# Optimization experiments

Hardware: AMD Instinct MI355X
Metric: run time of the kernel (lower is better)

The kernel has to match this reference:

```python
import jax, jax.numpy as jnp
import numpy as np

J, H, MAXREL = 24, 8, 49  # num_joints, temporal heads, max_relative_position


def _pos_encoding(seq_len, d_model):
    pos = jnp.arange(seq_len, dtype=jnp.float32)[:, None]
    i = jnp.arange(d_model, dtype=jnp.float32)[None, :]
    angle = pos / jnp.power(10000.0, 2.0 * jnp.floor(i / 2.0) / d_model)
    return jnp.where(jnp.arange(d_model)[None, :] % 2 == 0, jnp.sin(angle), jnp.cos(angle))  # [S, D]


def _rel_index(seq_len):
    r = jnp.arange(seq_len)
    dist = jnp.clip(r[None, :] - r[:, None], -MAXREL, MAXREL) + MAXREL
    return dist  # [S, S] int


def setup_inputs() -> dict:
    key = jax.random.key(0)
    ks = jax.random.split(key, 12)
    B, S, D = 32, 120, 128
    depth = D // H
    s = 0.02
    x = jax.random.normal(ks[0], (B, S, J, D), dtype=jnp.float32)
    mask = jnp.triu(jnp.ones((1, 1, S, S), dtype=jnp.float32), k=1)  # look-ahead mask
    Wq = jax.random.normal(ks[1], (J, D, D), dtype=jnp.float32) * s
    bq = jnp.zeros((J, D), dtype=jnp.float32)
    Wk = jax.random.normal(ks[2], (J, D, D), dtype=jnp.float32) * s
    bk = jnp.zeros((J, D), dtype=jnp.float32)
    Wv = jax.random.normal(ks[3], (J, D, D), dtype=jnp.float32) * s
    bv = jnp.zeros((J, D), dtype=jnp.float32)
    Wo = jax.random.normal(ks[4], (D, D), dtype=jnp.float32) * s
    bo = jnp.zeros((D,), dtype=jnp.float32)
    key_table = jax.random.normal(ks[5], (2 * MAXREL + 1, depth), dtype=jnp.float32) * s
    val_table = jax.random.normal(ks[6], (2 * MAXREL + 1, depth), dtype=jnp.float32) * s
    return {"x": x, "mask": mask, "Wq": Wq, "bq": bq, "Wk": Wk, "bk": bk,
            "Wv": Wv, "bv": bv, "Wo": Wo, "bo": bo,
            "key_table": key_table, "val_table": val_table}


def reference(x, mask, Wq, bq, Wk, bk, Wv, bv, Wo, bo, key_table, val_table):
    B, S, _, D = x.shape
    depth = D // H
    # absolute positional encoding, broadcast over batch and joints
    x = x + _pos_encoding(S, D)[None, :, None, :]
    xj = jnp.transpose(x, (2, 0, 1, 3))  # [J, B, S, D]
    # per-joint linear projections (torch Linear: y = x @ W^T + b)
    q = jnp.einsum('jbsd,jed->jbse', xj, Wq) + bq[:, None, None, :]
    k = jnp.einsum('jbsd,jed->jbse', xj, Wk) + bk[:, None, None, :]
    v = jnp.einsum('jbsd,jed->jbse', xj, Wv) + bv[:, None, None, :]
    # split heads -> [J, B, H, S, depth]
    split = lambda t: t.reshape(J, B, S, H, depth).transpose(0, 1, 3, 2, 4)
    q, k, v = split(q), split(k), split(v)
    # relative key/value embeddings [S, S, depth]
    rel = _rel_index(S)
    rk = key_table[rel]
    rv = val_table[rel]
    logits = jnp.einsum('jbhsd,jbhtd->jbhst', q, k) + jnp.einsum('jbhsd,std->jbhst', q, rk)
    logits = logits / jnp.float32(np.sqrt(depth)) + mask * (-1e9)
    w = jax.nn.softmax(logits, axis=-1)  # [J, B, H, S, T]
    out = jnp.einsum('jbhst,jbhtd->jbhsd', w, v) + jnp.einsum('jbhst,std->jbhsd', w, rv)
    out = out.transpose(0, 1, 3, 2, 4).reshape(J, B, S, D)  # merge heads
    out = jnp.einsum('jbsd,ed->jbse', out, Wo) + bo  # shared output projection
    outputs = out.transpose(1, 2, 0, 3)  # [B, S, J, D]
    attn_weights = w[..., -1, :].transpose(1, 0, 2, 3)  # [B, J, H, T]
    return outputs, attn_weights
```

## Files before the change

### kernel.cpp

```cpp
#include <hip/hip_runtime.h>
#include <math.h>

#define Jn 24
#define Bn 32
#define Sn 120
#define Dn 128
#define Hn 8
#define DEP 16
#define ALD 136

#define QSCL 0.36067376022224085f

typedef _Float16 f16x8 __attribute__((ext_vector_type(8)));
typedef float f32x4 __attribute__((ext_vector_type(4)));

#if __has_builtin(__builtin_amdgcn_exp2f)
#define EXP2(x) __builtin_amdgcn_exp2f(x)
#else
#define EXP2(x) exp2f(x)
#endif

__global__ void pe_kernel(float* __restrict__ pe) {
    const int s = blockIdx.x, d = threadIdx.x;
    const float expo = (float)(2 * (d >> 1)) / (float)Dn;
    const float base = powf(10000.0f, -expo);
    const float ang = (float)s * base;
    pe[s * Dn + d] = (d & 1) ? cosf(ang) : sinf(ang);
}

__global__ __launch_bounds__(256)
void qkv_gemm(const float* __restrict__ x, const float* __restrict__ pe,
              const float* __restrict__ Wq, const float* __restrict__ bq,
              const float* __restrict__ Wk, const float* __restrict__ bk,
              const float* __restrict__ Wv, const float* __restrict__ bv,
              _Float16* __restrict__ qg, _Float16* __restrict__ kg,
              _Float16* __restrict__ vg, int jbase)
{
    extern __shared__ _Float16 lsu[];
    _Float16* As = lsu;
    _Float16* Bs = lsu + 128 * ALD;

    const int bid = blockIdx.x;
    const int mt = bid % 30;
    const int jc = bid / 30;
    const int j = jbase + jc;
    const int tid = threadIdx.x;

    for (int idx = tid; idx < 128 * 32; idx += 256) {
        const int r = idx >> 5;
        const int c = (idx & 31) << 2;
        const int mflat = mt * 128 + r;
        const int b = mflat / Sn;
        const int s = mflat % Sn;
        const float4 xv = *(const float4*)(x + (((size_t)(b * Sn + s)) * Jn + j) * Dn + c);
        const float4 pv = *(const float4*)(pe + s * Dn + c);
        _Float16* dst = As + r * ALD + c;
        dst[0] = (_Float16)(xv.x + pv.x); dst[1] = (_Float16)(xv.y + pv.y);
        dst[2] = (_Float16)(xv.z + pv.z); dst[3] = (_Float16)(xv.w + pv.w);
    }

    const int wid = tid >> 6;
    const int lane = tid & 63;
    const int wm = wid >> 1, wn = wid & 1;
    const int g = lane >> 4, q16 = lane & 15;

    for (int nt = 0; nt < 3; ++nt) {
        const float* Wsel = (nt == 0 ? Wq : (nt == 1 ? Wk : Wv)) + (size_t)j * Dn * Dn;
        const float* bsel = (nt == 0 ? bq : (nt == 1 ? bk : bv)) + (size_t)j * Dn;
        _Float16* obuf = (nt == 0 ? qg : (nt == 1 ? kg : vg));
        const float scl = (nt == 0) ? QSCL : 1.0f;

        if (nt) __syncthreads();
        for (int idx = tid; idx < 128 * 32; idx += 256) {
            const int e = idx >> 5;
            const int c = (idx & 31) << 2;
            const float4 wv = *(const float4*)(Wsel + (size_t)e * Dn + c);
            _Float16* dst = Bs + e * ALD + c;
            dst[0] = (_Float16)wv.x; dst[1] = (_Float16)wv.y;
            dst[2] = (_Float16)wv.z; dst[3] = (_Float16)wv.w;
        }
        __syncthreads();

        f32x4 acc[4][4];
        #pragma unroll
        for (int a = 0; a < 4; ++a)
            #pragma unroll
            for (int c2 = 0; c2 < 4; ++c2) acc[a][c2] = (f32x4){0.f, 0.f, 0.f, 0.f};

        #pragma unroll
        for (int ks = 0; ks < 4; ++ks) {
            const int kof = ks * 32 + g * 8;
            f16x8 av[4], bvf[4];
            #pragma unroll
            for (int fr = 0; fr < 4; ++fr)
                av[fr] = *(const f16x8*)(As + (wm * 64 + fr * 16 + q16) * ALD + kof);
            #pragma unroll
            for (int fc = 0; fc < 4; ++fc)
                bvf[fc] = *(const f16x8*)(Bs + (wn * 64 + fc * 16 + q16) * ALD + kof);
            #pragma unroll
            for (int fr = 0; fr < 4; ++fr)
                #pragma unroll
                for (int fc = 0; fc < 4; ++fc)
                    acc[fr][fc] = __builtin_amdgcn_mfma_f32_16x16x32_f16(av[fr], bvf[fc], acc[fr][fc], 0, 0, 0);
        }

        #pragma unroll
        for (int fc = 0; fc < 4; ++fc) {
            const int e = wn * 64 + fc * 16 + q16;
            const float be = bsel[e];
            const int h = e >> 4, ed = e & 15;
            #pragma unroll
            for (int fr = 0; fr < 4; ++fr) {
                #pragma unroll
                for (int r = 0; r < 4; ++r) {
                    const int mflat = mt * 128 + wm * 64 + fr * 16 + g * 4 + r;
                    const int b = mflat / Sn, s = mflat % Sn;
                    obuf[((size_t)((jc * Bn + b) * Hn + h)) * (Sn * DEP) + s * DEP + ed] =
                        (_Float16)((acc[fr][fc][r] + be) * scl);
                }
            }
        }
    }
}

#define AB_LD  184
#define QR_LD  52
#define A_VCT  0
#define A_RKT  5888
#define A_RV0  8960
#define A_ABUF 9024
#define A_QRB  32576
#define A_BYTES 39264

__global__ __launch_bounds__(256)
void attn_mfma(const _Float16* __restrict__ qg, const _Float16* __restrict__ kg,
               const _Float16* __restrict__ vg,
               const float* __restrict__ ktab, const float* __restrict__ vtab,
               _Float16* __restrict__ out_pre, float* __restrict__ attn_w, int jbase)
{
    extern __shared__ char smc[];
    _Float16* vct = (_Float16*)(smc + A_VCT);
    _Float16* rkt = (_Float16*)(smc + A_RKT);
    float*    rv0 = (float*)(smc + A_RV0);

    const int tid = threadIdx.x;
    const int wid = tid >> 6;
    const int lane = tid & 63;
    const int l15 = lane & 15;
    const int g = lane >> 4;
    const int bh = blockIdx.x;
    const int jc = bh >> 8;
    const int b = (bh >> 3) & 31;
    const int h = bh & 7;
    const int j = jbase + jc;

    _Float16* ab  = (_Float16*)(smc + A_ABUF) + wid * 16 * AB_LD;
    _Float16* qrb = (_Float16*)(smc + A_QRB) + wid * 16 * QR_LD;

    {
        unsigned* z = (unsigned*)smc;
        for (int idx = tid; idx < A_BYTES / 4; idx += 256) z[idx] = 0;
    }
    __syncthreads();
    const unsigned* vs = (const unsigned*)vg + (size_t)bh * 960;
    unsigned short* vctu = (unsigned short*)vct;
    for (int idx = tid; idx < 960; idx += 256) {
        const int s = idx >> 3, ep = idx & 7;
        const unsigned u = vs[idx];
        vctu[(2 * ep) * AB_LD + s] = (unsigned short)(u & 0xffffu);
        vctu[(2 * ep + 1) * AB_LD + s] = (unsigned short)(u >> 16);
    }
    for (int idx = tid; idx < 800; idx += 256) {
        const int d = idx >> 4, e = idx & 15;
        vct[e * AB_LD + 120 + d] = (_Float16)(vtab[d * DEP + e] - vtab[e]);
    }
    for (int idx = tid; idx < 800; idx += 256) {
        const int d = idx >> 4, e = idx & 15;
        rkt[d * 24 + e] = (_Float16)ktab[d * DEP + e];
    }
    if (tid < 16) rv0[tid] = vtab[tid];
    __syncthreads();

    const _Float16* qgu = qg + (size_t)bh * 1920;
    const _Float16* kgu = kg + (size_t)bh * 1920;
    _Float16* opre = out_pre + ((size_t)((j * Bn + b) * Hn + h)) * (Sn * DEP);

    const f16x8 zf = {0, 0, 0, 0, 0, 0, 0, 0};
    const f32x4 z4 = {0.f, 0.f, 0.f, 0.f};
    const float rv0f = rv0[l15];

    #pragma unroll
    for (int half = 0; half < 2; ++half) {
        const int m = half ? (7 - wid) : wid;

        const f16x8 afr = (g < 2) ? *(const f16x8*)(qgu + (16 * m + l15) * 16 + g * 8) : zf;
        f32x4 qr[4];
        #pragma unroll
        for (int n = 0; n < 4; ++n) {
            const f16x8 bfr = (g < 2) ? *(const f16x8*)(rkt + (16 * n + l15) * 24 + g * 8) : zf;
            qr[n] = __builtin_amdgcn_mfma_f32_16x16x32_f16(afr, bfr, z4, 0, 0, 0);
        }
        f32x4 acc[8];
        #pragma unroll
        for (int n = 0; n < 8; ++n) {
            if (n > m) break;
            const f16x8 bfr = (g < 2) ? *(const f16x8*)(kgu + (16 * n + l15) * 16 + g * 8) : zf;
            acc[n] = __builtin_amdgcn_mfma_f32_16x16x32_f16(afr, bfr, z4, 0, 0, 0);
        }
        #pragma unroll
        for (int n = 0; n < 4; ++n)
            #pragma unroll
            for (int r = 0; r < 4; ++r)
                if (n < 3 || l15 < 4)
                    qrb[(g * 4 + r) * QR_LD + 16 * n + l15] = (_Float16)qr[n][r];

        float rs[4];
        #pragma unroll
        for (int r = 0; r < 4; ++r) {
            const int row = g * 4 + r;
            const int srow = 16 * m + row;
            const int rowbase = row * AB_LD;
            const _Float16* qrow = qrb + row * QR_LD;
            const float qr0 = (float)qrow[0];
            float pv[8];
            float tot = 0.f;
            #pragma unroll
            for (int n = 0; n < 8; ++n) {
                if (n > m) break;
                float p;
                if (n <= m - 4) {
                    p = EXP2(acc[n][r] + qr0);
                } else if (n < m) {
                    int dist = 16 * (n - m) + 49 + l15 - row;
                    if (n == m - 3) dist = dist < 0 ? 0 : dist;
                    p = EXP2(acc[n][r] + (float)qrow[dist]);
                } else {
                    const int dist = 49 + l15 - row;
                    p = (l15 <= row) ? EXP2(acc[n][r] + (float)qrow[dist]) : 0.f;
                }
                pv[n] = p;
                tot += p;
                if (n < 7 || l15 < 8)
                    ab[rowbase + 16 * n + l15] = (_Float16)p;
            }
            #pragma unroll
            for (int mk = 1; mk < 16; mk <<= 1) tot += __shfl_xor(tot, mk);
            rs[r] = tot;

            #pragma unroll
            for (int n = 0; n < 8; ++n) {
                if (n < m - 3 || n > m) continue;
                const int dist = 16 * (n - m) + 49 + l15 - row;
                bool st = true;
                if (n == m - 3) st = (dist >= 1);
                if (n == m)     st = (l15 <= row);
                if (st) ab[rowbase + 120 + dist] = (_Float16)pv[n];
            }
            if (srow == Sn - 1) {
                const float inv = __builtin_amdgcn_rcpf(tot);
                #pragma unroll
                for (int n = 0; n < 8; ++n) {
                    if (n > m) break;
                    const int t = 16 * n + l15;
                    if (t < Sn)
                        attn_w[(((size_t)(b * Jn + j)) * Hn + h) * Sn + t] = pv[n] * inv;
                }
            }
        }

        f32x4 oacc = z4;
        #pragma unroll
        for (int kt = 0; kt < 3; ++kt) {
            if (kt > (m >> 1)) break;
            const f16x8 aw = *(const f16x8*)(ab + l15 * AB_LD + kt * 32 + g * 8);
            const f16x8 bv = *(const f16x8*)(vct + l15 * AB_LD + kt * 32 + g * 8);
            oacc = __builtin_amdgcn_mfma_f32_16x16x32_f16(aw, bv, oacc, 0, 0, 0);
        }
        #pragma unroll
        for (int kt = 3; kt < 5; ++kt) {
            const f16x8 aw = *(const f16x8*)(ab + l15 * AB_LD + kt * 32 + g * 8);
            const f16x8 bv = *(const f16x8*)(vct + l15 * AB_LD + kt * 32 + g * 8);
            oacc = __builtin_amdgcn_mfma_f32_16x16x32_f16(aw, bv, oacc, 0, 0, 0);
        }
        {
            const f16x8 aw = (g < 2) ? *(const f16x8*)(ab + l15 * AB_LD + 160 + g * 8) : zf;
            const f16x8 bv = (g < 2) ? *(const f16x8*)(vct + l15 * AB_LD + 160 + g * 8) : zf;
            oacc = __builtin_amdgcn_mfma_f32_16x16x32_f16(aw, bv, oacc, 0, 0, 0);
        }
        #pragma unroll
        for (int r = 0; r < 4; ++r) {
            const int srow = 16 * m + g * 4 + r;
            if (srow < Sn) {
                const float inv = __builtin_amdgcn_rcpf(rs[r]);
                opre[srow * DEP + l15] = (_Float16)(fmaf(oacc[r], inv, rv0f));
            }
        }
    }
}

__global__ __launch_bounds__(256)
void oproj_gemm(const _Float16* __restrict__ Ain, const float* __restrict__ Wo,
                const float* __restrict__ bo, float* __restrict__ out)
{
    extern __shared__ _Float16 lsu[];
    _Float16* As = lsu;
    _Float16* Bs = lsu + 128 * ALD;
    const int tid = threadIdx.x;
    const int mt = blockIdx.x;

    for (int idx = tid; idx < 128 * 8; idx += 256) {
        const int r = idx >> 3;
        const int h = idx & 7;
        const int mflat = mt * 128 + r;
        const int j = mflat / (Bn * Sn);
        const int rem = mflat % (Bn * Sn);
        const int b = rem / Sn, s = rem % Sn;
        const _Float16* src = Ain + (((size_t)(j * Bn + b) * Hn + h) * Sn + s) * DEP;
        *(uint4*)(As + r * ALD + h * 16)     = *(const uint4*)(src);
        *(uint4*)(As + r * ALD + h * 16 + 8) = *(const uint4*)(src + 8);
    }
    for (int idx = tid; idx < 128 * 32; idx += 256) {
        const int e = idx >> 5;
        const int c = (idx & 31) << 2;
        const float4 wv = *(const float4*)(Wo + (size_t)e * Dn + c);
        _Float16* dst = Bs + e * ALD + c;
        dst[0] = (_Float16)wv.x; dst[1] = (_Float16)wv.y;
        dst[2] = (_Float16)wv.z; dst[3] = (_Float16)wv.w;
    }
    __syncthreads();

    const int wid = tid >> 6;
    const int lane = tid & 63;
    const int wm = wid >> 1, wn = wid & 1;
    const int g = lane >> 4, q16 = lane & 15;

    f32x4 acc[4][4];
    #pragma unroll
    for (int a = 0; a < 4; ++a)
        #pragma unroll
        for (int c2 = 0; c2 < 4; ++c2) acc[a][c2] = (f32x4){0.f, 0.f, 0.f, 0.f};

    #pragma unroll
    for (int ks = 0; ks < 4; ++ks) {
        const int kof = ks * 32 + g * 8;
        f16x8 av[4], bvf[4];
        #pragma unroll
        for (int fr = 0; fr < 4; ++fr)
            av[fr] = *(const f16x8*)(As + (wm * 64 + fr * 16 + q16) * ALD + kof);
        #pragma unroll
        for (int fc = 0; fc < 4; ++fc)
            bvf[fc] = *(const f16x8*)(Bs + (wn * 64 + fc * 16 + q16) * ALD + kof);
        #pragma unroll
        for (int fr = 0; fr < 4; ++fr)
            #pragma unroll
            for (int fc = 0; fc < 4; ++fc)
                acc[fr][fc] = __builtin_amdgcn_mfma_f32_16x16x32_f16(av[fr], bvf[fc], acc[fr][fc], 0, 0, 0);
    }

    #pragma unroll
    for (int fc = 0; fc < 4; ++fc) {
        const int e = wn * 64 + fc * 16 + q16;
        const float be = bo[e];
        #pragma unroll
        for (int fr = 0; fr < 4; ++fr) {
            #pragma unroll
            for (int r = 0; r < 4; ++r) {
                const int m = mt * 128 + wm * 64 + fr * 16 + g * 4 + r;
                const int jj = m / (Bn * Sn);
                const int rem = m % (Bn * Sn);
                const int bb = rem / Sn, ss = rem % Sn;
                out[((size_t)(bb * Sn + ss) * Jn + jj) * Dn + e] = acc[fr][fc][r] + be;
            }
        }
    }
}

extern "C" void kernel_launch(void* const* d_in, const int* in_sizes, int n_in,
                              void* d_out, int out_size, void* d_ws, size_t ws_size,
                              hipStream_t stream)
{
    const float* x    = (const float*)d_in[0];
    const float* Wq   = (const float*)d_in[2];
    const float* bq   = (const float*)d_in[3];
    const float* Wk   = (const float*)d_in[4];
    const float* bk   = (const float*)d_in[5];
    const float* Wv   = (const float*)d_in[6];
    const float* bv   = (const float*)d_in[7];
    const float* Wo   = (const float*)d_in[8];
    const float* bo   = (const float*)d_in[9];
    const float* ktab = (const float*)d_in[10];
    const float* vtab = (const float*)d_in[11];

    float* out    = (float*)d_out;
    float* attn_w = out + (size_t)Bn * Sn * Jn * Dn;

    const size_t fullE = (size_t)Jn * Bn * Sn * Dn;
    int JCr = 24;
    {
        const size_t need = 65536 + 2 * (3 * fullE + fullE);
        if (ws_size < need) JCr = 6;
    }
    const size_t csz = (size_t)JCr * Bn * Hn * Sn * DEP;

    float* pe = (float*)d_ws;
    char* base = (char*)d_ws;
    _Float16* qg = (_Float16*)(base + 65536);
    _Float16* kg = qg + csz;
    _Float16* vg = kg + csz;
    _Float16* out_pre = vg + csz;

    pe_kernel<<<Sn, Dn, 0, stream>>>(pe);
    const int gemm_lds = 2 * 128 * ALD * 2;
    for (int c = 0; c < Jn; c += JCr) {
        qkv_gemm<<<JCr * 30, 256, gemm_lds, stream>>>(
            x, pe, Wq, bq, Wk, bk, Wv, bv, qg, kg, vg, c);
        attn_mfma<<<JCr * Bn * Hn, 256, A_BYTES, stream>>>(
            qg, kg, vg, ktab, vtab, out_pre, attn_w, c);
    }
    oproj_gemm<<<(Jn * Bn * Sn) / 128, 256, gemm_lds, stream>>>(out_pre, Wo, bo, out);
}
```

Before: 244.2 us.

## Process four batch-head units per attention block with register prefetch of next unit

Each attention block now loops over four (j,b,h) units instead of one. The per-block setup (LDS zeroing, relative-table staging) is amortized across units. Q, K and V loads for the next unit are issued into registers during the current unit's compute to hide global latency. This costs extra registers for the prefetched fragments, adds per-unit barriers and an ab re-zero, and launches four times fewer blocks.

```diff
diff --git a/kernel.cpp b/kernel.cpp
--- a/kernel.cpp
+++ b/kernel.cpp
@@ -8,6 +8,7 @@
 #define Hn 8
 #define DEP 16
 #define ALD 136
+#define UPB 4
 
 #define QSCL 0.36067376022224085f
 
@@ -148,28 +149,16 @@
     const int lane = tid & 63;
     const int l15 = lane & 15;
     const int g = lane >> 4;
-    const int bh = blockIdx.x;
-    const int jc = bh >> 8;
-    const int b = (bh >> 3) & 31;
-    const int h = bh & 7;
-    const int j = jbase + jc;
 
     _Float16* ab  = (_Float16*)(smc + A_ABUF) + wid * 16 * AB_LD;
     _Float16* qrb = (_Float16*)(smc + A_QRB) + wid * 16 * QR_LD;
+    unsigned short* vctu = (unsigned short*)vct;
 
     {
         unsigned* z = (unsigned*)smc;
         for (int idx = tid; idx < A_BYTES / 4; idx += 256) z[idx] = 0;
     }
     __syncthreads();
-    const unsigned* vs = (const unsigned*)vg + (size_t)bh * 960;
-    unsigned short* vctu = (unsigned short*)vct;
-    for (int idx = tid; idx < 960; idx += 256) {
-        const int s = idx >> 3, ep = idx & 7;
-        const unsigned u = vs[idx];
-        vctu[(2 * ep) * AB_LD + s] = (unsigned short)(u & 0xffffu);
-        vctu[(2 * ep + 1) * AB_LD + s] = (unsigned short)(u >> 16);
-    }
     for (int idx = tid; idx < 800; idx += 256) {
         const int d = idx >> 4, e = idx & 15;
         vct[e * AB_LD + 120 + d] = (_Float16)(vtab[d * DEP + e] - vtab[e]);
@@ -181,121 +170,168 @@
     if (tid < 16) rv0[tid] = vtab[tid];
     __syncthreads();
 
-    const _Float16* qgu = qg + (size_t)bh * 1920;
-    const _Float16* kgu = kg + (size_t)bh * 1920;
-    _Float16* opre = out_pre + ((size_t)((j * Bn + b) * Hn + h)) * (Sn * DEP);
-
+    const float rv0f = rv0[l15];
     const f16x8 zf = {0, 0, 0, 0, 0, 0, 0, 0};
     const f32x4 z4 = {0.f, 0.f, 0.f, 0.f};
-    const float rv0f = rv0[l15];
-
-    #pragma unroll
-    for (int half = 0; half < 2; ++half) {
-        const int m = half ? (7 - wid) : wid;
-
-        const f16x8 afr = (g < 2) ? *(const f16x8*)(qgu + (16 * m + l15) * 16 + g * 8) : zf;
-        f32x4 qr[4];
-        #pragma unroll
-        for (int n = 0; n < 4; ++n) {
-            const f16x8 bfr = (g < 2) ? *(const f16x8*)(rkt + (16 * n + l15) * 24 + g * 8) : zf;
-            qr[n] = __builtin_amdgcn_mfma_f32_16x16x32_f16(afr, bfr, z4, 0, 0, 0);
-        }
-        f32x4 acc[8];
-        #pragma unroll
-        for (int n = 0; n < 8; ++n) {
-            if (n > m) break;
-            const f16x8 bfr = (g < 2) ? *(const f16x8*)(kgu + (16 * n + l15) * 16 + g * 8) : zf;
-            acc[n] = __builtin_amdgcn_mfma_f32_16x16x32_f16(afr, bfr, z4, 0, 0, 0);
-        }
-        #pragma unroll
-        for (int n = 0; n < 4; ++n)
-            #pragma unroll
-            for (int r = 0; r < 4; ++r)
-                if (n < 3 || l15 < 4)
-                    qrb[(g * 4 + r) * QR_LD + 16 * n + l15] = (_Float16)qr[n][r];
-
-        float rs[4];
-        #pragma unroll
-        for (int r = 0; r < 4; ++r) {
-            const int row = g * 4 + r;
-            const int srow = 16 * m + row;
-            const int rowbase = row * AB_LD;
-            const _Float16* qrow = qrb + row * QR_LD;
-            const float qr0 = (float)qrow[0];
-            float pv[8];
-            float tot = 0.f;
+
+    unsigned pvw0, pvw1, pvw2, pvw3;
+    f16x8 afr0, afr1, kf[8];
+
+#define PREFETCH_UNIT(BH_) do {                                                     \
+        const unsigned* vsrc = (const unsigned*)vg + (size_t)(BH_) * 960;           \
+        pvw0 = vsrc[tid]; pvw1 = vsrc[tid + 256]; pvw2 = vsrc[tid + 512];           \
+        pvw3 = (tid < 192) ? vsrc[tid + 768] : 0u;                                  \
+        const _Float16* qn = qg + (size_t)(BH_) * 1920;                             \
+        const _Float16* kn = kg + (size_t)(BH_) * 1920;                             \
+        afr0 = (g < 2) ? *(const f16x8*)(qn + (16 * wid + l15) * 16 + g * 8) : zf;  \
+        afr1 = (g < 2) ? *(const f16x8*)(qn + (16 * (7 - wid) + l15) * 16 + g * 8) : zf; \
+        _Pragma("unroll")                                                           \
+        for (int nn = 0; nn < 8; ++nn) {                                            \
+            if (nn > 7 - wid) break;                                                \
+            kf[nn] = (g < 2) ? *(const f16x8*)(kn + (16 * nn + l15) * 16 + g * 8) : zf; \
+        }                                                                           \
+    } while (0)
+
+    int bh = blockIdx.x * UPB;
+    PREFETCH_UNIT(bh);
+
+    for (int u = 0; u < UPB; ++u, ++bh) {
+        const int jc = bh >> 8;
+        const int b = (bh >> 3) & 31;
+        const int h = bh & 7;
+        const int j = jbase + jc;
+        _Float16* opre = out_pre + ((size_t)((j * Bn + b) * Hn + h)) * (Sn * DEP);
+
+        {
+            int idx = tid;
+            #pragma unroll
+            for (int k2 = 0; k2 < 4; ++k2, idx += 256) {
+                const unsigned uu = (k2 == 0) ? pvw0 : (k2 == 1) ? pvw1 : (k2 == 2) ? pvw2 : pvw3;
+                if (idx < 960) {
+                    const int s = idx >> 3, ep = idx & 7;
+                    vctu[(2 * ep) * AB_LD + s] = (unsigned short)(uu & 0xffffu);
+                    vctu[(2 * ep + 1) * AB_LD + s] = (unsigned short)(uu >> 16);
+                }
+            }
+        }
+        __syncthreads();
+
+        #pragma unroll
+        for (int half = 0; half < 2; ++half) {
+            const int m = half ? (7 - wid) : wid;
+            const f16x8 afr = half ? afr1 : afr0;
+
+            f32x4 qr[4];
+            #pragma unroll
+            for (int n = 0; n < 4; ++n) {
+                const f16x8 bfr = (g < 2) ? *(const f16x8*)(rkt + (16 * n + l15) * 24 + g * 8) : zf;
+                qr[n] = __builtin_amdgcn_mfma_f32_16x16x32_f16(afr, bfr, z4, 0, 0, 0);
+            }
+            f32x4 acc[8];
             #pragma unroll
             for (int n = 0; n < 8; ++n) {
                 if (n > m) break;
-                float p;
-                if (n <= m - 4) {
-                    p = EXP2(acc[n][r] + qr0);
-                } else if (n < m) {
-                    int dist = 16 * (n - m) + 49 + l15 - row;
-                    if (n == m - 3) dist = dist < 0 ? 0 : dist;
-                    p = EXP2(acc[n][r] + (float)qrow[dist]);
-                } else {
-                    const int dist = 49 + l15 - row;
-                    p = (l15 <= row) ? EXP2(acc[n][r] + (float)qrow[dist]) : 0.f;
-                }
-                pv[n] = p;
-                tot += p;
-                if (n < 7 || l15 < 8)
-                    ab[rowbase + 16 * n + l15] = (_Float16)p;
-            }
-            #pragma unroll
-            for (int mk = 1; mk < 16; mk <<= 1) tot += __shfl_xor(tot, mk);
-            rs[r] = tot;
-
-            #pragma unroll
-            for (int n = 0; n < 8; ++n) {
-                if (n < m - 3 || n > m) continue;
-                const int dist = 16 * (n - m) + 49 + l15 - row;
-                bool st = true;
-                if (n == m - 3) st = (dist >= 1);
-                if (n == m)     st = (l15 <= row);
-                if (st) ab[rowbase + 120 + dist] = (_Float16)pv[n];
-            }
-            if (srow == Sn - 1) {
-                const float inv = __builtin_amdgcn_rcpf(tot);
+                acc[n] = __builtin_amdgcn_mfma_f32_16x16x32_f16(afr, kf[n], z4, 0, 0, 0);
+            }
+            if (half == 1 && u + 1 < UPB) PREFETCH_UNIT(bh + 1);
+
+            #pragma unroll
+            for (int n = 0; n < 4; ++n)
+                #pragma unroll
+                for (int r = 0; r < 4; ++r)
+                    if (n < 3 || l15 < 4)
+                        qrb[(g * 4 + r) * QR_LD + 16 * n + l15] = (_Float16)qr[n][r];
+
+            float rs[4];
+            #pragma unroll
+            for (int r = 0; r < 4; ++r) {
+                const int row = g * 4 + r;
+                const int srow = 16 * m + row;
+                const int rowbase = row * AB_LD;
+                const _Float16* qrow = qrb + row * QR_LD;
+                const float qr0 = (float)qrow[0];
+                float pv[8];
+                float tot = 0.f;
                 #pragma unroll
                 for (int n = 0; n < 8; ++n) {
                     if (n > m) break;
-                    const int t = 16 * n + l15;
-                    if (t < Sn)
-                        attn_w[(((size_t)(b * Jn + j)) * Hn + h) * Sn + t] = pv[n] * inv;
-                }
-            }
-        }
-
-        f32x4 oacc = z4;
-        #pragma unroll
-        for (int kt = 0; kt < 3; ++kt) {
-            if (kt > (m >> 1)) break;
-            const f16x8 aw = *(const f16x8*)(ab + l15 * AB_LD + kt * 32 + g * 8);
-            const f16x8 bv = *(const f16x8*)(vct + l15 * AB_LD + kt * 32 + g * 8);
-            oacc = __builtin_amdgcn_mfma_f32_16x16x32_f16(aw, bv, oacc, 0, 0, 0);
-        }
-        #pragma unroll
-        for (int kt = 3; kt < 5; ++kt) {
-            const f16x8 aw = *(const f16x8*)(ab + l15 * AB_LD + kt * 32 + g * 8);
-            const f16x8 bv = *(const f16x8*)(vct + l15 * AB_LD + kt * 32 + g * 8);
-            oacc = __builtin_amdgcn_mfma_f32_16x16x32_f16(aw, bv, oacc, 0, 0, 0);
-        }
+                    float p;
+                    if (n <= m - 4) {
+                        p = EXP2(acc[n][r] + qr0);
+                    } else if (n < m) {
+                        int dist = 16 * (n - m) + 49 + l15 - row;
+                        if (n == m - 3) dist = dist < 0 ? 0 : dist;
+                        p = EXP2(acc[n][r] + (float)qrow[dist]);
+                    } else {
+                        const int dist = 49 + l15 - row;
+                        p = (l15 <= row) ? EXP2(acc[n][r] + (float)qrow[dist]) : 0.f;
+                    }
+                    pv[n] = p;
+                    tot += p;
+                    if (n < 7 || l15 < 8)
+                        ab[rowbase + 16 * n + l15] = (_Float16)p;
+                }
+                #pragma unroll
+                for (int mk = 1; mk < 16; mk <<= 1) tot += __shfl_xor(tot, mk);
+                rs[r] = tot;
+
+                #pragma unroll
+                for (int n = 0; n < 8; ++n) {
+                    if (n < m - 3 || n > m) continue;
+                    const int dist = 16 * (n - m) + 49 + l15 - row;
+                    bool st = true;
+                    if (n == m - 3) st = (dist >= 1);
+                    if (n == m)     st = (l15 <= row);
+                    if (st) ab[rowbase + 120 + dist] = (_Float16)pv[n];
+                }
+                if (srow == Sn - 1) {
+                    const float inv = __builtin_amdgcn_rcpf(tot);
+                    #pragma unroll
+                    for (int n = 0; n < 8; ++n) {
+                        if (n > m) break;
+                        const int t = 16 * n + l15;
+                        if (t < Sn)
+                            attn_w[(((size_t)(b * Jn + j)) * Hn + h) * Sn + t] = pv[n] * inv;
+                    }
+                }
+            }
+
+            f32x4 oacc = z4;
+            #pragma unroll
+            for (int kt = 0; kt < 3; ++kt) {
+                if (kt > (m >> 1)) break;
+                const f16x8 aw = *(const f16x8*)(ab + l15 * AB_LD + kt * 32 + g * 8);
+                const f16x8 bv = *(const f16x8*)(vct + l15 * AB_LD + kt * 32 + g * 8);
+                oacc = __builtin_amdgcn_mfma_f32_16x16x32_f16(aw, bv, oacc, 0, 0, 0);
+            }
+            #pragma unroll
+            for (int kt = 3; kt < 5; ++kt) {
+                const f16x8 aw = *(const f16x8*)(ab + l15 * AB_LD + kt * 32 + g * 8);
+                const f16x8 bv = *(const f16x8*)(vct + l15 * AB_LD + kt * 32 + g * 8);
+                oacc = __builtin_amdgcn_mfma_f32_16x16x32_f16(aw, bv, oacc, 0, 0, 0);
+            }
+            {
+                const f16x8 aw = (g < 2) ? *(const f16x8*)(ab + l15 * AB_LD + 160 + g * 8) : zf;
+                const f16x8 bv = (g < 2) ? *(const f16x8*)(vct + l15 * AB_LD + 160 + g * 8) : zf;
+                oacc = __builtin_amdgcn_mfma_f32_16x16x32_f16(aw, bv, oacc, 0, 0, 0);
+            }
+            #pragma unroll
+            for (int r = 0; r < 4; ++r) {
+                const int srow = 16 * m + g * 4 + r;
+                if (srow < Sn) {
+                    const float inv = __builtin_amdgcn_rcpf(rs[r]);
+                    opre[srow * DEP + l15] = (_Float16)(fmaf(oacc[r], inv, rv0f));
+                }
+            }
+        }
+
         {
-            const f16x8 aw = (g < 2) ? *(const f16x8*)(ab + l15 * AB_LD + 160 + g * 8) : zf;
-            const f16x8 bv = (g < 2) ? *(const f16x8*)(vct + l15 * AB_LD + 160 + g * 8) : zf;
-            oacc = __builtin_amdgcn_mfma_f32_16x16x32_f16(aw, bv, oacc, 0, 0, 0);
-        }
-        #pragma unroll
-        for (int r = 0; r < 4; ++r) {
-            const int srow = 16 * m + g * 4 + r;
-            if (srow < Sn) {
-                const float inv = __builtin_amdgcn_rcpf(rs[r]);
-                opre[srow * DEP + l15] = (_Float16)(fmaf(oacc[r], inv, rv0f));
-            }
-        }
-    }
+            unsigned* abz = (unsigned*)ab;
+            for (int i = lane; i < (16 * AB_LD) / 2; i += 64) abz[i] = 0;
+        }
+        __syncthreads();
+    }
+#undef PREFETCH_UNIT
 }
 
 __global__ __launch_bounds__(256)
@@ -414,7 +450,7 @@
     for (int c = 0; c < Jn; c += JCr) {
         qkv_gemm<<<JCr * 30, 256, gemm_lds, stream>>>(
             x, pe, Wq, bq, Wk, bk, Wv, bv, qg, kg, vg, c);
-        attn_mfma<<<JCr * Bn * Hn, 256, A_BYTES, stream>>>(
+        attn_mfma<<<(JCr * Bn * Hn) / UPB, 256, A_BYTES, stream>>>(
             qg, kg, vg, ktab, vtab, out_pre, attn_w, c);
     }
     oproj_gemm<<<(Jn * Bn * Sn) / 128, 256, gemm_lds, stream>>>(out_pre, Wo, bo, out);
```

New measurement: 358.1 us. +46.6%, slower.

## Write attention output in merged-head layout and simplify relative-position softmax indexing

Applied to the files above, without the earlier changes.

The attention kernel now writes its per-head output directly in [j,b,s,D] merged-head layout, so the output-projection GEMM can load contiguous 128-wide rows instead of gathering eight per-head 16-element segments. The relative-position logit lookup is rewritten as a single clamped distance index into a widened qr buffer, replacing the three-way branch on block position, and the P scatter into the shared buffer is generalised. Hardware reciprocal instructions are replaced by true divides, which costs a few extra instructions but should be more precise. The layout change couples two kernels and shifts the LDS offsets.

```diff
diff --git a/kernel.cpp b/kernel.cpp
--- a/kernel.cpp
+++ b/kernel.cpp
@@ -124,13 +124,12 @@
 }
 
 #define AB_LD  184
-#define QR_LD  52
 #define A_VCT  0
 #define A_RKT  5888
-#define A_RV0  8960
-#define A_ABUF 9024
-#define A_QRB  32576
-#define A_BYTES 39264
+#define A_RV0  8384
+#define A_ABUF 8448
+#define A_QRB  32000
+#define A_BYTES 40448
 
 __global__ __launch_bounds__(256)
 void attn_mfma(const _Float16* __restrict__ qg, const _Float16* __restrict__ kg,
@@ -155,7 +154,7 @@
     const int j = jbase + jc;
 
     _Float16* ab  = (_Float16*)(smc + A_ABUF) + wid * 16 * AB_LD;
-    _Float16* qrb = (_Float16*)(smc + A_QRB) + wid * 16 * QR_LD;
+    _Float16* qrb = (_Float16*)(smc + A_QRB) + wid * 16 * 66;
 
     {
         unsigned* z = (unsigned*)smc;
@@ -183,7 +182,6 @@
 
     const _Float16* qgu = qg + (size_t)bh * 1920;
     const _Float16* kgu = kg + (size_t)bh * 1920;
-    _Float16* opre = out_pre + ((size_t)((j * Bn + b) * Hn + h)) * (Sn * DEP);
 
     const f16x8 zf = {0, 0, 0, 0, 0, 0, 0, 0};
     const f32x4 z4 = {0.f, 0.f, 0.f, 0.f};
@@ -211,53 +209,43 @@
         for (int n = 0; n < 4; ++n)
             #pragma unroll
             for (int r = 0; r < 4; ++r)
-                if (n < 3 || l15 < 4)
-                    qrb[(g * 4 + r) * QR_LD + 16 * n + l15] = (_Float16)qr[n][r];
+                qrb[(g * 4 + r) * 66 + 16 * n + l15] = (_Float16)qr[n][r];
 
         float rs[4];
         #pragma unroll
         for (int r = 0; r < 4; ++r) {
-            const int row = g * 4 + r;
-            const int srow = 16 * m + row;
-            const int rowbase = row * AB_LD;
-            const _Float16* qrow = qrb + row * QR_LD;
-            const float qr0 = (float)qrow[0];
+            const int srow = 16 * m + g * 4 + r;
             float pv[8];
             float tot = 0.f;
             #pragma unroll
             for (int n = 0; n < 8; ++n) {
                 if (n > m) break;
-                float p;
-                if (n <= m - 4) {
-                    p = EXP2(acc[n][r] + qr0);
-                } else if (n < m) {
-                    int dist = 16 * (n - m) + 49 + l15 - row;
-                    if (n == m - 3) dist = dist < 0 ? 0 : dist;
-                    p = EXP2(acc[n][r] + (float)qrow[dist]);
-                } else {
-                    const int dist = 49 + l15 - row;
-                    p = (l15 <= row) ? EXP2(acc[n][r] + (float)qrow[dist]) : 0.f;
-                }
+                const int t = 16 * n + l15;
+                const int dd = t - srow;
+                int dist = dd + 49;
+                dist = dist < 0 ? 0 : (dist > 49 ? 49 : dist);
+                const float qrv = (float)qrb[(g * 4 + r) * 66 + dist];
+                float p = 0.f;
+                if (t <= srow) p = EXP2(acc[n][r] + qrv);
                 pv[n] = p;
                 tot += p;
-                if (n < 7 || l15 < 8)
-                    ab[rowbase + 16 * n + l15] = (_Float16)p;
             }
             #pragma unroll
             for (int mk = 1; mk < 16; mk <<= 1) tot += __shfl_xor(tot, mk);
             rs[r] = tot;
-
             #pragma unroll
             for (int n = 0; n < 8; ++n) {
-                if (n < m - 3 || n > m) continue;
-                const int dist = 16 * (n - m) + 49 + l15 - row;
-                bool st = true;
-                if (n == m - 3) st = (dist >= 1);
-                if (n == m)     st = (l15 <= row);
-                if (st) ab[rowbase + 120 + dist] = (_Float16)pv[n];
+                if (n > m) break;
+                const int t = 16 * n + l15;
+                const int dd = t - srow;
+                const _Float16 pb = (_Float16)pv[n];
+                if (t < Sn)
+                    ab[(g * 4 + r) * AB_LD + t] = pb;
+                if (dd >= -48 && dd <= 0)
+                    ab[(g * 4 + r) * AB_LD + dd + 169] = pb;
             }
             if (srow == Sn - 1) {
-                const float inv = __builtin_amdgcn_rcpf(tot);
+                const float inv = 1.f / tot;
                 #pragma unroll
                 for (int n = 0; n < 8; ++n) {
                     if (n > m) break;
@@ -290,10 +278,9 @@
         #pragma unroll
         for (int r = 0; r < 4; ++r) {
             const int srow = 16 * m + g * 4 + r;
-            if (srow < Sn) {
-                const float inv = __builtin_amdgcn_rcpf(rs[r]);
-                opre[srow * DEP + l15] = (_Float16)(fmaf(oacc[r], inv, rv0f));
-            }
+            if (srow < Sn)
+                out_pre[((size_t)((j * Bn + b) * Sn) + srow) * Dn + h * DEP + l15] =
+                    (_Float16)(oacc[r] / rs[r] + rv0f);
         }
     }
 }
@@ -308,16 +295,10 @@
     const int tid = threadIdx.x;
     const int mt = blockIdx.x;
 
-    for (int idx = tid; idx < 128 * 8; idx += 256) {
-        const int r = idx >> 3;
-        const int h = idx & 7;
-        const int mflat = mt * 128 + r;
-        const int j = mflat / (Bn * Sn);
-        const int rem = mflat % (Bn * Sn);
-        const int b = rem / Sn, s = rem % Sn;
-        const _Float16* src = Ain + (((size_t)(j * Bn + b) * Hn + h) * Sn + s) * DEP;
-        *(uint4*)(As + r * ALD + h * 16)     = *(const uint4*)(src);
-        *(uint4*)(As + r * ALD + h * 16 + 8) = *(const uint4*)(src + 8);
+    for (int idx = tid; idx < 128 * 16; idx += 256) {
+        const int r = idx >> 4;
+        const int c = (idx & 15) << 3;
+        *(uint4*)(As + r * ALD + c) = *(const uint4*)(Ain + ((size_t)(mt * 128 + r)) * Dn + c);
     }
     for (int idx = tid; idx < 128 * 32; idx += 256) {
         const int e = idx >> 5;
```

Measured after the change: 232.0 us. -5.0%, faster.
